# Kernel tuning notes

Measured on AMD Instinct MI355X. Metric: run time of the kernel, lower is better.

## Reference

```python
import jax, jax.numpy as jnp
import numpy as np

# ---- config (matches init_kwargs) ----
B, NP, DIM, HEADS, DH, NDIM = 32, 576, 512, 8, 64, 16
N = NP + 1                 # seq len incl cls token = 577
INNER = HEADS * DH         # 512


def setup_inputs() -> dict:
    key = jax.random.key(0)
    ks = jax.random.split(key, 11)
    D2 = 2 * DIM  # bidirectional EMA doubles kernel dim
    return {
        "x": jax.random.normal(ks[0], (B, N, DIM), jnp.float32),
        "W_qk": jax.random.normal(ks[1], (DIM, 2 * INNER), jnp.float32) / np.float32(np.sqrt(DIM)),
        "W_v": jax.random.normal(ks[2], (DIM, INNER), jnp.float32) / np.float32(np.sqrt(DIM)),
        "W_out": jax.random.normal(ks[3], (INNER, DIM), jnp.float32) / np.float32(np.sqrt(INNER)),
        "b_out": jnp.zeros((DIM,), jnp.float32),
        "rel_bias": jax.random.normal(ks[4], (2 * N - 1,), jnp.float32) * 0.02,
        "ema_delta": jax.random.normal(ks[5], (D2, NDIM, 1), jnp.float32),
        "ema_alpha": jax.random.normal(ks[6], (D2, NDIM, 1), jnp.float32),
        "ema_beta": jax.random.normal(ks[7], (D2, NDIM, 1), jnp.float32) * 0.5,
        "ema_gamma": jax.random.normal(ks[8], (D2, NDIM), jnp.float32) * 0.5,
        "ema_omega": jax.random.normal(ks[9], (DIM,), jnp.float32),
    }


def _ema_move(x, delta, alpha, beta, gamma, omega):
    """Bidirectional MultiHeadEMA (MEGA) via FFT convolution. x: (B, L, D)."""
    b, L, d = x.shape
    scale = jnp.asarray(np.sqrt(1.0 / NDIM), x.dtype)
    p = jax.nn.sigmoid(delta)                      # (2D, N, 1)
    q = 1.0 - p * jax.nn.sigmoid(alpha)            # (2D, N, 1), in (0,1)
    vander = jnp.arange(L, dtype=x.dtype)[None, None, :] * jnp.log(q)  # (2D, N, L)
    kern = (p * beta) * jnp.exp(vander)            # (2D, N, L)
    k = jnp.einsum('dnl,dn->dl', kern, gamma * scale)  # (2D, L)
    k1, k2 = k[:d], k[d:]
    # combined bidirectional kernel, length 2L-1
    kk = jnp.pad(k1, ((0, 0), (L - 1, 0))) + jnp.pad(k2[:, ::-1], ((0, 0), (0, L - 1)))
    xt = jnp.pad(x.transpose(0, 2, 1), ((0, 0), (0, 0), (L - 1, 0)))  # (B, D, 2L-1)
    fft_len = 2 * L - 1
    nfft = 2 * fft_len
    out = jnp.fft.irfft(jnp.fft.rfft(xt, n=nfft) * jnp.fft.rfft(kk, n=nfft)[None], n=nfft)
    s = 2 * L - 2
    out = out[..., s:s + L].transpose(0, 2, 1).astype(x.dtype)  # (B, L, D)
    return jax.nn.silu(out + x * omega)


def _rel_pos_bias(rb, seq_len):
    """RelativePositionalBias (MEGA): (2*N-1,) param -> (seq_len, seq_len) bias."""
    max_pos = N
    bvec = rb[max_pos - seq_len: max_pos + seq_len - 1]   # (2*seq_len-1,)
    t = jnp.pad(bvec, (0, seq_len))
    t = jnp.tile(t, seq_len)[:-seq_len].reshape(seq_len, 3 * seq_len - 2)
    r = (2 * seq_len - 1) // 2
    return t[:, r:t.shape[1] - r]


def reference(x, W_qk, W_v, W_out, b_out, rel_bias,
              ema_delta, ema_alpha, ema_beta, ema_gamma, ema_omega):
    b, n, _ = x.shape
    cls_tok = x[:, :1]
    moved = _ema_move(x[:, 1:], ema_delta, ema_alpha, ema_beta, ema_gamma, ema_omega)
    xm = jnp.concatenate([cls_tok, moved], axis=1)        # (B, N, DIM)
    q, k = jnp.split(xm @ W_qk, 2, axis=-1)
    v = xm @ W_v                                          # smooth_v_as_well=True

    def heads(t):
        return t.reshape(b, n, HEADS, DH).transpose(0, 2, 1, 3)  # (B, H, N, DH)

    q, k, v = heads(q), heads(k), heads(v)
    dots = jnp.einsum('bhid,bhjd->bhij', q, k) * (DH ** -0.5)
    attn = jax.nn.softmax(dots, axis=-1)
    attn = attn + _rel_pos_bias(rel_bias, n)[None, None]  # bias added AFTER softmax
    out = jnp.einsum('bhij,bhjd->bhid', attn, v)
    out = out.transpose(0, 2, 1, 3).reshape(b, n, INNER)
    return out @ W_out + b_out
```

## Files before the change

kernel.cpp:

```cpp
#include <hip/hip_runtime.h>

typedef unsigned short ushort;

typedef __bf16 bf16x8 __attribute__((ext_vector_type(8)));
typedef float  f32x4  __attribute__((ext_vector_type(4)));
typedef unsigned short u16x8 __attribute__((ext_vector_type(8)));
typedef unsigned short u16x4 __attribute__((ext_vector_type(4)));
typedef unsigned int   u32x2 __attribute__((ext_vector_type(2)));

static constexpr int BB   = 32;
static constexpr int NN   = 577;
static constexpr int LL   = 576;
static constexpr int DIMC = 512;
static constexpr int BN   = BB * NN;

static constexpr size_t SZ_WQKVT = 1536ull * 512 * 2;
static constexpr size_t SZ_WOUTT = 512ull * 512 * 2;
static constexpr size_t SZ_QK    = (size_t)BN * 1024 * 2;
static constexpr size_t SZ_V     = (size_t)BN * 512 * 2;
static constexpr size_t SZ_VT    = 256ull * 64 * 640 * 2;
static constexpr size_t OFF_WQKVT = 0;
static constexpr size_t OFF_WOUTT = OFF_WQKVT + SZ_WQKVT;
static constexpr size_t OFF_QTAB  = OFF_WOUTT + SZ_WOUTT;
static constexpr size_t OFF_CTAB  = OFF_QTAB + 65536;
static constexpr size_t OFF_QK    = OFF_CTAB + 65536;
static constexpr size_t OFF_V     = OFF_QK + SZ_QK;
static constexpr size_t OFF_REGION= OFF_V + SZ_V;
static constexpr size_t OFF_XM    = OFF_REGION;
static constexpr size_t OFF_VT    = OFF_REGION;
static constexpr size_t OFF_AO    = OFF_REGION + SZ_VT;
static constexpr size_t OFF_ST    = OFF_AO;
static constexpr size_t WS_NEEDED = OFF_AO + SZ_V;

__device__ __forceinline__ ushort bf16bits(float f) {
  unsigned int u = __builtin_bit_cast(unsigned int, f);
  u = (u + 0x7fffu + ((u >> 16) & 1u)) >> 16;
  return (ushort)u;
}
__device__ __forceinline__ float sigmoidf_(float z) { return 1.f / (1.f + __expf(-z)); }
__device__ __forceinline__ float siluf(float z)     { return z / (1.f + __expf(-z)); }

__global__ __launch_bounds__(256) void k_prep(
    const float* __restrict__ delta, const float* __restrict__ alpha,
    const float* __restrict__ beta,  const float* __restrict__ gamma,
    const float* __restrict__ Wqk,   const float* __restrict__ Wv,
    const float* __restrict__ Wout,
    float* __restrict__ qtab, float* __restrict__ ctab,
    ushort* __restrict__ Wqkvt, ushort* __restrict__ Woutt)
{
  int idx = blockIdx.x * 256 + threadIdx.x;
  if (idx < 16384) {
    float p = sigmoidf_(delta[idx]);
    float q = 1.f - p * sigmoidf_(alpha[idx]);
    qtab[idx] = q;
    ctab[idx] = p * beta[idx] * gamma[idx] * 0.25f;
  }
  int i2 = idx - 16384;
  if (i2 >= 0 && i2 < 1536 * 512) {
    int n = i2 >> 9, k = i2 & 511;
    float w = (n < 1024) ? Wqk[k * 1024 + n] : Wv[k * 512 + (n - 1024)];
    Wqkvt[i2] = bf16bits(w);
  }
  int i3 = i2 - 1536 * 512;
  if (i3 >= 0 && i3 < 512 * 512) {
    int n = i3 >> 9, k = i3 & 511;
    Woutt[i3] = bf16bits(Wout[k * 512 + n]);
  }
}


__global__ __launch_bounds__(64) void k_ema_p1(
    const float* __restrict__ x, const float* __restrict__ qtab,
    float* __restrict__ st)
{
  const int gx = blockIdx.x, cy = blockIdx.y, b = blockIdx.z;
  if (gx < 8) {
    const int d = gx * 64 + threadIdx.x;
    float q[16], h[16];
    #pragma unroll
    for (int n = 0; n < 16; ++n) { q[n] = qtab[d*16+n]; h[n] = 0.f; }
    const float* xp = x + ((size_t)b * NN + 1) * DIMC + d;
    const int blo = cy * 9;
    float xn[8];
    #pragma unroll
    for (int u = 0; u < 8; ++u) xn[u] = xp[(blo * 8 + u) * DIMC];
    for (int blk = blo; blk < blo + 9; ++blk) {
      float xv[8];
      #pragma unroll
      for (int u = 0; u < 8; ++u) xv[u] = xn[u];
      if (blk < blo + 8) {
        #pragma unroll
        for (int u = 0; u < 8; ++u) xn[u] = xp[((blk + 1) * 8 + u) * DIMC];
      }
      #pragma unroll
      for (int u = 0; u < 8; ++u) {
        float xx = xv[u];
        #pragma unroll
        for (int n = 0; n < 16; ++n) h[n] = fmaf(q[n], h[n], xx);
      }
    }
    float* sp = st + (((size_t)b * 8 + cy) * 16) * 512 + d;
    #pragma unroll
    for (int n = 0; n < 16; ++n) sp[n * 512] = h[n];
  } else {
    const int d = (gx - 8) * 64 + threadIdx.x;
    float q[16], g[16];
    #pragma unroll
    for (int n = 0; n < 16; ++n) { q[n] = qtab[(d+512)*16+n]; g[n] = 0.f; }
    const float* xp = x + ((size_t)b * NN + 1) * DIMC + d;
    const int blo = (7 - cy) * 9;
    float xn[8];
    #pragma unroll
    for (int u = 0; u < 8; ++u) xn[u] = xp[((blo + 8) * 8 + u) * DIMC];
    for (int blk = blo + 8; blk >= blo; --blk) {
      float xv[8];
      #pragma unroll
      for (int u = 0; u < 8; ++u) xv[u] = xn[u];
      if (blk > blo) {
        #pragma unroll
        for (int u = 0; u < 8; ++u) xn[u] = xp[((blk - 1) * 8 + u) * DIMC];
      }
      #pragma unroll
      for (int u = 7; u >= 0; --u) {
        float xx = xv[u];
        #pragma unroll
        for (int n = 0; n < 16; ++n) g[n] = fmaf(q[n], g[n], xx);
      }
    }
    float* sp = st + (((size_t)(32 + b) * 8 + cy) * 16) * 512 + d;
    #pragma unroll
    for (int n = 0; n < 16; ++n) sp[n * 512] = g[n];
  }
}

__global__ __launch_bounds__(256) void k_ema_mid(
    const float* __restrict__ qtab, float* __restrict__ st)
{
  int idx = blockIdx.x * 256 + threadIdx.x;
  int d = idx & 511;
  int rest = idx >> 9;
  int n = rest & 15;
  int db = rest >> 4;
  int dir = db >> 5;
  float q = qtab[(((size_t)dir << 9) + d) * 16 + n];
  float q2 = q * q, q4 = q2 * q2, q8 = q4 * q4;
  float q16 = q8 * q8, q32 = q16 * q16, q64 = q32 * q32;
  float qL = q64 * q8;
  float h = 0.f;
  float* sp = st + ((size_t)db * 128 + n) * 512 + d;
  #pragma unroll
  for (int c = 0; c < 8; ++c) {
    float tmp = (c < 7) ? sp[c * 8192] : 0.f;
    sp[c * 8192] = h;
    h = fmaf(qL, h, tmp);
  }
}

__global__ __launch_bounds__(64) void k_ema_p3(
    const float* __restrict__ x, const float* __restrict__ qtab,
    const float* __restrict__ ctab, const float* __restrict__ st,
    float* __restrict__ y1, float* __restrict__ y2)
{
  const int gx = blockIdx.x, cy = blockIdx.y, b = blockIdx.z;
  if (gx < 8) {
    const int d = gx * 64 + threadIdx.x;
    float q[16], c[16], h[16];
    const float* sp = st + (((size_t)b * 8 + cy) * 16) * 512 + d;
    #pragma unroll
    for (int n = 0; n < 16; ++n) { q[n] = qtab[d*16+n]; c[n] = ctab[d*16+n]; h[n] = sp[n*512]; }
    const float* xp = x  + ((size_t)b * NN + 1) * DIMC + d;
    float*       yp = y1 + ((size_t)b * LL)     * DIMC + d;
    const int blo = cy * 9;
    float xn[8];
    #pragma unroll
    for (int u = 0; u < 8; ++u) xn[u] = xp[(blo * 8 + u) * DIMC];
    for (int blk = blo; blk < blo + 9; ++blk) {
      float xv[8];
      #pragma unroll
      for (int u = 0; u < 8; ++u) xv[u] = xn[u];
      if (blk < blo + 8) {
        #pragma unroll
        for (int u = 0; u < 8; ++u) xn[u] = xp[((blk + 1) * 8 + u) * DIMC];
      }
      #pragma unroll
      for (int u = 0; u < 8; ++u) {
        float xx = xv[u], y = 0.f;
        #pragma unroll
        for (int n = 0; n < 16; ++n) { h[n] = fmaf(q[n], h[n], xx); y = fmaf(c[n], h[n], y); }
        yp[(blk * 8 + u) * DIMC] = y;
      }
    }
  } else {
    const int d = (gx - 8) * 64 + threadIdx.x;
    float q[16], c[16], g[16];
    const float* sp = st + (((size_t)(32 + b) * 8 + cy) * 16) * 512 + d;
    #pragma unroll
    for (int n = 0; n < 16; ++n) { q[n] = qtab[(d+512)*16+n]; c[n] = ctab[(d+512)*16+n]; g[n] = sp[n*512]; }
    const float* xp = x  + ((size_t)b * NN + 1) * DIMC + d;
    float*       yp = y2 + ((size_t)b * LL)     * DIMC + d;
    const int blo = (7 - cy) * 9;
    float xn[8];
    #pragma unroll
    for (int u = 0; u < 8; ++u) xn[u] = xp[((blo + 8) * 8 + u) * DIMC];
    for (int blk = blo + 8; blk >= blo; --blk) {
      float xv[8];
      #pragma unroll
      for (int u = 0; u < 8; ++u) xv[u] = xn[u];
      if (blk > blo) {
        #pragma unroll
        for (int u = 0; u < 8; ++u) xn[u] = xp[((blk - 1) * 8 + u) * DIMC];
      }
      #pragma unroll
      for (int u = 7; u >= 0; --u) {
        float xx = xv[u], y = 0.f;
        #pragma unroll
        for (int n = 0; n < 16; ++n) { g[n] = fmaf(q[n], g[n], xx); y = fmaf(c[n], g[n], y); }
        yp[(blk * 8 + u) * DIMC] = y;
      }
    }
  }
}

__global__ __launch_bounds__(256) void k_ema_comb(
    const float* __restrict__ x, const float* __restrict__ y1,
    const float* __restrict__ y2, const float* __restrict__ omega,
    ushort* __restrict__ xm)
{
  size_t v = (size_t)blockIdx.x * 256 + threadIdx.x;
  size_t e = v * 4;
  int n = (int)(e >> 9);
  int d = (int)(e & 511);
  int b = n / 577;
  int i = n - b * 577;
  f32x4 xv = *(const f32x4*)(x + e);
  u16x4 o;
  if (i == 0) {
    #pragma unroll
    for (int k = 0; k < 4; ++k) o[k] = bf16bits(xv[k]);
  } else {
    size_t ey = ((size_t)b * LL + (i - 1)) * DIMC + d;
    f32x4 a  = *(const f32x4*)(y1 + ey);
    f32x4 c2 = *(const f32x4*)(y2 + ey);
    f32x4 om = *(const f32x4*)(omega + d);
    #pragma unroll
    for (int k = 0; k < 4; ++k) o[k] = bf16bits(siluf(a[k] + c2[k] + xv[k] * om[k]));
  }
  *(u16x4*)(xm + e) = o;
}

__global__ __launch_bounds__(256) void k_qkv(
    const ushort* __restrict__ A, const ushort* __restrict__ Bt,
    ushort* __restrict__ qk, ushort* __restrict__ v)
{
  __shared__ alignas(16) ushort lA[128 * 40];
  __shared__ alignas(16) ushort lB[128 * 40];
  const int tid = threadIdx.x, wv = tid >> 6, lane = tid & 63;
  const int quad = lane >> 4, c16 = lane & 15;
  const int fid = blockIdx.y * 12 + blockIdx.x;
  const int xcd = fid & 7, ord = fid >> 3;
  const int wg  = (xcd < 4 ? xcd * 218 : 872 + (xcd - 4) * 217) + ord;
  const int row0 = (wg / 12) * 128, n0 = (wg % 12) * 128;
  const int wm = (wv >> 1) * 64, wn = (wv & 1) * 64;
  f32x4 z4 = {0.f, 0.f, 0.f, 0.f};
  f32x4 acc[4][4];
  #pragma unroll
  for (int mi = 0; mi < 4; ++mi)
    #pragma unroll
    for (int ni = 0; ni < 4; ++ni) acc[mi][ni] = z4;

  for (int kt = 0; kt < 16; ++kt) {
    const int k0 = kt * 32;
    u16x8 sa[2], sb[2];
    #pragma unroll
    for (int it = 0; it < 2; ++it) {
      int ch = it * 256 + tid;
      int r = ch >> 2, cc = ch & 3;
      int grow = row0 + r; if (grow > BN - 1) grow = BN - 1;
      sa[it] = *(const u16x8*)(A + (size_t)grow * 512 + k0 + cc * 8);
      sb[it] = *(const u16x8*)(Bt + (size_t)(n0 + r) * 512 + k0 + cc * 8);
    }
    __syncthreads();
    #pragma unroll
    for (int it = 0; it < 2; ++it) {
      int ch = it * 256 + tid;
      int r = ch >> 2, cc = ch & 3;
      *(u16x8*)(lA + r * 40 + cc * 8) = sa[it];
      *(u16x8*)(lB + r * 40 + cc * 8) = sb[it];
    }
    __syncthreads();
    bf16x8 af[4], bfv[4];
    #pragma unroll
    for (int mi = 0; mi < 4; ++mi)
      af[mi] = *(const bf16x8*)(lA + (wm + mi * 16 + c16) * 40 + quad * 8);
    #pragma unroll
    for (int ni = 0; ni < 4; ++ni)
      bfv[ni] = *(const bf16x8*)(lB + (wn + ni * 16 + c16) * 40 + quad * 8);
    #pragma unroll
    for (int mi = 0; mi < 4; ++mi)
      #pragma unroll
      for (int ni = 0; ni < 4; ++ni)
        acc[mi][ni] = __builtin_amdgcn_mfma_f32_16x16x32_bf16(af[mi], bfv[ni], acc[mi][ni], 0, 0, 0);
  }
  const bool isv = (n0 >= 1024);
  const float osc = (n0 < 512) ? 0.125f : 1.0f;
  #pragma unroll
  for (int mi = 0; mi < 4; ++mi) {
    #pragma unroll
    for (int r = 0; r < 4; ++r) {
      int grow = row0 + wm + mi * 16 + quad * 4 + r;
      if (grow < BN) {
        #pragma unroll
        for (int ni = 0; ni < 4; ++ni) {
          int col = n0 + wn + ni * 16 + c16;
          ushort vb = bf16bits(acc[mi][ni][r] * osc);
          if (!isv) qk[(size_t)grow * 1024 + col] = vb;
          else      v[(size_t)grow * 512 + (col - 1024)] = vb;
        }
      }
    }
  }
}

__global__ __launch_bounds__(256) void k_vtrans(
    const ushort* __restrict__ v, ushort* __restrict__ vt)
{
  __shared__ alignas(16) ushort lt[64 * 72];
  const int tid = threadIdx.x;
  const int bh = blockIdx.y, b = bh >> 3, h = bh & 7;
  const int j0 = blockIdx.x * 64;
  #pragma unroll
  for (int pass = 0; pass < 2; ++pass) {
    int cch = pass * 256 + tid;
    int jl = cch >> 3, cc = cch & 7;
    int gj = j0 + jl;
    u16x8 val = {0, 0, 0, 0, 0, 0, 0, 0};
    if (gj < 577) val = *(const u16x8*)(v + ((size_t)(b * NN + gj)) * 512 + h * 64 + cc * 8);
    *(u16x8*)(lt + jl * 72 + cc * 8) = val;
  }
  __syncthreads();
  #pragma unroll
  for (int pass = 0; pass < 2; ++pass) {
    int cch = pass * 256 + tid;
    int dh = cch >> 3, jc = cch & 7;
    u16x8 o;
    #pragma unroll
    for (int e = 0; e < 8; ++e) o[e] = lt[(jc * 8 + e) * 72 + dh];
    *(u16x8*)(vt + ((size_t)(bh * 64 + dh)) * 640 + j0 + jc * 8) = o;
  }
}

__global__ __launch_bounds__(256) void k_fattn(
    const ushort* __restrict__ qk, const ushort* __restrict__ vt,
    const float* __restrict__ relb, ushort* __restrict__ ao)
{
  __shared__ alignas(16) ushort lk[64 * 64];
  __shared__ alignas(16) ushort lv[64 * 64];
  __shared__ alignas(16) ushort lp[128 * 64];
  __shared__ ushort lbias16[1280];
  const int tid = threadIdx.x, wv = tid >> 6, lane = tid & 63;
  const int quad = lane >> 4, c16 = lane & 15;
  const int bh = blockIdx.x, b = bh >> 3, h = bh & 7;
  const int i0 = blockIdx.y * 128, wm = wv * 32;
  for (int t = tid; t < 1280; t += 256) {
    int idx = t - 64;
    lbias16[t] = (idx >= 0 && idx < 1153) ? bf16bits(relb[idx]) : (ushort)0;
  }
  bf16x8 aq[2][2];
  #pragma unroll
  for (int ms = 0; ms < 2; ++ms) {
    int gi = i0 + wm + ms * 16 + c16; if (gi > 576) gi = 576;
    const ushort* qp = qk + ((size_t)(b * NN + gi)) * 1024 + h * 64;
    #pragma unroll
    for (int kk = 0; kk < 2; ++kk)
      aq[ms][kk] = *(const bf16x8*)(qp + (kk * 4 + quad) * 8);
  }
  const int s_r = tid >> 3, s_c = tid & 7;
  const ushort* kbase = qk + ((size_t)b * NN) * 1024 + 512 + h * 64 + s_c * 8;
  const ushort* vbase = vt + ((size_t)bh * 64) * 640 + s_c * 8;

  float lsum[2] = {0.f, 0.f};
  f32x4 z4 = {0.f, 0.f, 0.f, 0.f};
  f32x4 accp[2][4], accb[2][4];
  #pragma unroll
  for (int ms = 0; ms < 2; ++ms)
    #pragma unroll
    for (int ns = 0; ns < 4; ++ns) { accp[ms][ns] = z4; accb[ms][ns] = z4; }

  u16x8 sk[2], sv[2];
  #pragma unroll
  for (int it = 0; it < 2; ++it) {
    int r = it * 32 + s_r;
    sk[it] = *(const u16x8*)(kbase + (size_t)r * 1024);
    sv[it] = *(const u16x8*)(vbase + (size_t)r * 640);
  }

  for (int jt = 0; jt < 10; ++jt) {
    __syncthreads();
    #pragma unroll
    for (int it = 0; it < 2; ++it) {
      int r = it * 32 + s_r;
      int pc = (s_c ^ (r & 7)) * 8;
      *(u16x8*)(lk + r * 64 + pc) = sk[it];
      *(u16x8*)(lv + r * 64 + pc) = sv[it];
    }
    __syncthreads();
    #pragma unroll
    for (int ms = 0; ms < 2; ++ms) {
      f32x4 dacc[4] = {z4, z4, z4, z4};
      #pragma unroll
      for (int kk = 0; kk < 2; ++kk) {
        const int ck = kk * 4 + quad;
        #pragma unroll
        for (int ns = 0; ns < 4; ++ns) {
          const int row = ns * 16 + c16;
          bf16x8 bk = *(const bf16x8*)(lk + row * 64 + ((ck ^ (row & 7)) * 8));
          dacc[ns] = __builtin_amdgcn_mfma_f32_16x16x32_bf16(bk, aq[ms][kk], dacc[ns], 0, 0, 0);
        }
      }
      const int irow = wm + ms * 16 + c16;
      const int xr = irow & 7;
      #pragma unroll
      for (int ns = 0; ns < 4; ++ns) {
        float ex[4];
        #pragma unroll
        for (int r = 0; r < 4; ++r) {
          float e = __expf(dacc[ns][r]);
          if (jt == 9 && (ns * 16 + quad * 4 + r) >= 1) e = 0.f;
          ex[r] = e;
        }
        lsum[ms] += (ex[0] + ex[1]) + (ex[2] + ex[3]);
        unsigned int p0 = (unsigned int)bf16bits(ex[0]) | ((unsigned int)bf16bits(ex[1]) << 16);
        unsigned int p1 = (unsigned int)bf16bits(ex[2]) | ((unsigned int)bf16bits(ex[3]) << 16);
        u32x2 pw = {p0, p1};
        const int lc = ns * 2 + (quad >> 1);
        *(u32x2*)(lp + irow * 64 + ((lc ^ xr) * 8) + (quad & 1) * 4) = pw;
      }
    }
    __syncthreads();
    if (jt < 9) {
      const int j0n = (jt + 1) * 64;
      #pragma unroll
      for (int it = 0; it < 2; ++it) {
        int r = it * 32 + s_r;
        int gj = j0n + r; if (gj > 576) gj = 576;
        sk[it] = *(const u16x8*)(kbase + (size_t)gj * 1024);
        sv[it] = *(const u16x8*)(vbase + (size_t)r * 640 + j0n);
      }
    }
    const int j0 = jt * 64;
    #pragma unroll
    for (int kk = 0; kk < 2; ++kk) {
      const int ck = kk * 4 + quad;
      bf16x8 ap[2], ab[2];
      #pragma unroll
      for (int ms = 0; ms < 2; ++ms) {
        const int row = wm + ms * 16 + c16;
        ap[ms] = *(const bf16x8*)(lp + row * 64 + ((ck ^ (row & 7)) * 8));
        u16x8 abu;
        const int base = 64 + 576 + j0 + kk * 32 + quad * 8 - (i0 + row);
        #pragma unroll
        for (int e = 0; e < 8; ++e) abu[e] = lbias16[base + e];
        ab[ms] = __builtin_bit_cast(bf16x8, abu);
      }
      #pragma unroll
      for (int ns = 0; ns < 4; ++ns) {
        const int row = ns * 16 + c16;
        bf16x8 bV = *(const bf16x8*)(lv + row * 64 + ((ck ^ (row & 7)) * 8));
        #pragma unroll
        for (int ms = 0; ms < 2; ++ms) {
          accp[ms][ns] = __builtin_amdgcn_mfma_f32_16x16x32_bf16(ap[ms], bV, accp[ms][ns], 0, 0, 0);
          accb[ms][ns] = __builtin_amdgcn_mfma_f32_16x16x32_bf16(ab[ms], bV, accb[ms][ns], 0, 0, 0);
        }
      }
    }
  }
  float tot[2];
  #pragma unroll
  for (int ms = 0; ms < 2; ++ms) {
    float t = lsum[ms];
    t += __shfl_xor(t, 16);
    t += __shfl_xor(t, 32);
    tot[ms] = t;
  }
  #pragma unroll
  for (int ms = 0; ms < 2; ++ms) {
    #pragma unroll
    for (int r = 0; r < 4; ++r) {
      float li = 1.f / __shfl(tot[ms], quad * 4 + r);
      int ii = i0 + wm + ms * 16 + quad * 4 + r;
      if (ii < 577) {
        #pragma unroll
        for (int ns = 0; ns < 4; ++ns)
          ao[((size_t)(b * NN + ii)) * 512 + h * 64 + ns * 16 + c16] =
              bf16bits(accp[ms][ns][r] * li + accb[ms][ns][r]);
      }
    }
  }
}

__global__ __launch_bounds__(256) void k_out(
    const ushort* __restrict__ A, const ushort* __restrict__ Bt,
    const float* __restrict__ bout, float* __restrict__ out)
{
  __shared__ alignas(16) ushort lA[128 * 40];
  __shared__ alignas(16) ushort lB[128 * 40];
  const int tid = threadIdx.x, wv = tid >> 6, lane = tid & 63;
  const int quad = lane >> 4, c16 = lane & 15;
  const int row0 = blockIdx.y * 128, n0 = blockIdx.x * 128;
  const int wm = (wv >> 1) * 64, wn = (wv & 1) * 64;
  f32x4 z4 = {0.f, 0.f, 0.f, 0.f};
  f32x4 acc[4][4];
  #pragma unroll
  for (int mi = 0; mi < 4; ++mi)
    #pragma unroll
    for (int ni = 0; ni < 4; ++ni) acc[mi][ni] = z4;

  for (int kt = 0; kt < 16; ++kt) {
    const int k0 = kt * 32;
    u16x8 sa[2], sb[2];
    #pragma unroll
    for (int it = 0; it < 2; ++it) {
      int ch = it * 256 + tid;
      int r = ch >> 2, cc = ch & 3;
      int grow = row0 + r; if (grow > BN - 1) grow = BN - 1;
      sa[it] = *(const u16x8*)(A + (size_t)grow * 512 + k0 + cc * 8);
      sb[it] = *(const u16x8*)(Bt + (size_t)(n0 + r) * 512 + k0 + cc * 8);
    }
    __syncthreads();
    #pragma unroll
    for (int it = 0; it < 2; ++it) {
      int ch = it * 256 + tid;
      int r = ch >> 2, cc = ch & 3;
      *(u16x8*)(lA + r * 40 + cc * 8) = sa[it];
      *(u16x8*)(lB + r * 40 + cc * 8) = sb[it];
    }
    __syncthreads();
    bf16x8 af[4], bfv[4];
    #pragma unroll
    for (int mi = 0; mi < 4; ++mi)
      af[mi] = *(const bf16x8*)(lA + (wm + mi * 16 + c16) * 40 + quad * 8);
    #pragma unroll
    for (int ni = 0; ni < 4; ++ni)
      bfv[ni] = *(const bf16x8*)(lB + (wn + ni * 16 + c16) * 40 + quad * 8);
    #pragma unroll
    for (int mi = 0; mi < 4; ++mi)
      #pragma unroll
      for (int ni = 0; ni < 4; ++ni)
        acc[mi][ni] = __builtin_amdgcn_mfma_f32_16x16x32_bf16(af[mi], bfv[ni], acc[mi][ni], 0, 0, 0);
  }
  #pragma unroll
  for (int mi = 0; mi < 4; ++mi) {
    #pragma unroll
    for (int r = 0; r < 4; ++r) {
      int grow = row0 + wm + mi * 16 + quad * 4 + r;
      if (grow < BN) {
        #pragma unroll
        for (int ni = 0; ni < 4; ++ni) {
          int col = n0 + wn + ni * 16 + c16;
          out[(size_t)grow * 512 + col] = acc[mi][ni][r] + bout[col];
        }
      }
    }
  }
}

extern "C" void kernel_launch(void* const* d_in, const int* in_sizes, int n_in,
                              void* d_out, int out_size, void* d_ws, size_t ws_size,
                              hipStream_t stream) {
  (void)in_sizes; (void)n_in; (void)out_size;
  if (ws_size < WS_NEEDED) return;
  const float* x    = (const float*)d_in[0];
  const float* Wqk  = (const float*)d_in[1];
  const float* Wv   = (const float*)d_in[2];
  const float* Wout = (const float*)d_in[3];
  const float* bout = (const float*)d_in[4];
  const float* relb = (const float*)d_in[5];
  const float* edel = (const float*)d_in[6];
  const float* ealp = (const float*)d_in[7];
  const float* ebet = (const float*)d_in[8];
  const float* egam = (const float*)d_in[9];
  const float* eome = (const float*)d_in[10];

  char* ws = (char*)d_ws;
  ushort* Wqkvt = (ushort*)(ws + OFF_WQKVT);
  ushort* Woutt = (ushort*)(ws + OFF_WOUTT);
  float*  qtab  = (float*)(ws + OFF_QTAB);
  float*  ctab  = (float*)(ws + OFF_CTAB);
  ushort* qkb   = (ushort*)(ws + OFF_QK);
  ushort* vb    = (ushort*)(ws + OFF_V);
  ushort* xm    = (ushort*)(ws + OFF_XM);
  ushort* vtb   = (ushort*)(ws + OFF_VT);
  ushort* aob   = (ushort*)(ws + OFF_AO);
  float*  stf   = (float*)(ws + OFF_ST);
  float*  outp  = (float*)d_out;
  float*  y1    = outp;
  float*  y2    = (float*)(ws + OFF_QK);

  k_prep<<<dim3(4160), dim3(256), 0, stream>>>(edel, ealp, ebet, egam, Wqk, Wv, Wout,
                                               qtab, ctab, Wqkvt, Woutt);
  k_ema_p1<<<dim3(16, 7, 32), dim3(64), 0, stream>>>(x, qtab, stf);
  k_ema_mid<<<dim3(2048), dim3(256), 0, stream>>>(qtab, stf);
  k_ema_p3<<<dim3(16, 8, 32), dim3(64), 0, stream>>>(x, qtab, ctab, stf, y1, y2);
  k_ema_comb<<<dim3(9232), dim3(256), 0, stream>>>(x, y1, y2, eome, xm);
  k_qkv<<<dim3(12, 145), dim3(256), 0, stream>>>(xm, Wqkvt, qkb, vb);
  k_vtrans<<<dim3(10, 256), dim3(256), 0, stream>>>(vb, vtb);
  k_fattn<<<dim3(256, 5), dim3(256), 0, stream>>>(qkb, vtb, relb, aob);
  k_out<<<dim3(4, 145), dim3(256), 0, stream>>>(aob, Woutt, bout, outp);
}
```

Baseline: 324.6 us.

## Fuse bidirectional EMA scans with combine step and use exp2 softmax

Merges the forward and backward EMA scan kernel with the combine kernel. Each block now runs the backward scan into an fp16 shared buffer, then runs the forward scan and writes silu(y1+y2+x*omega) straight to bf16 xm. This removes the fp32 y1/y2 round trip through global memory and one launch, but halves the block count, serialises the two scans inside each block, and stores one scan direction in fp16. It also folds log2(e) into the Q scale so the attention kernel can use exp2, and moves the next K/V tile prefetch earlier, dropping one barrier.

```diff
diff --git a/kernel.cpp b/kernel.cpp
--- a/kernel.cpp
+++ b/kernel.cpp
@@ -156,29 +156,65 @@
   }
 }
 
-__global__ __launch_bounds__(64) void k_ema_p3(
+__global__ __launch_bounds__(64) void k_ema_fuse(
     const float* __restrict__ x, const float* __restrict__ qtab,
     const float* __restrict__ ctab, const float* __restrict__ st,
-    float* __restrict__ y1, float* __restrict__ y2)
-{
+    const float* __restrict__ omega, ushort* __restrict__ xm)
+{
+  __shared__ _Float16 yb[72 * 64];
+  const int lane = threadIdx.x;
   const int gx = blockIdx.x, cy = blockIdx.y, b = blockIdx.z;
-  if (gx < 8) {
-    const int d = gx * 64 + threadIdx.x;
+  const int d = gx * 64 + lane;
+  const float* xp = x + ((size_t)b * NN + 1 + cy * 72) * DIMC + d;
+  {
+    float q[16], c[16], g[16];
+    const float* sp = st + (((size_t)(32 + b) * 8 + (7 - cy)) * 16) * 512 + d;
+    #pragma unroll
+    for (int n = 0; n < 16; ++n) {
+      q[n] = qtab[(d + 512) * 16 + n];
+      c[n] = ctab[(d + 512) * 16 + n];
+      g[n] = sp[n * 512];
+    }
+    float xn[8];
+    #pragma unroll
+    for (int u = 0; u < 8; ++u) xn[u] = xp[(64 + u) * DIMC];
+    for (int blk = 8; blk >= 0; --blk) {
+      float xv[8];
+      #pragma unroll
+      for (int u = 0; u < 8; ++u) xv[u] = xn[u];
+      if (blk > 0) {
+        #pragma unroll
+        for (int u = 0; u < 8; ++u) xn[u] = xp[((blk - 1) * 8 + u) * DIMC];
+      }
+      #pragma unroll
+      for (int u = 7; u >= 0; --u) {
+        float xx = xv[u], y = 0.f;
+        #pragma unroll
+        for (int n = 0; n < 16; ++n) { g[n] = fmaf(q[n], g[n], xx); y = fmaf(c[n], g[n], y); }
+        yb[(blk * 8 + u) * 64 + lane] = (_Float16)y;
+      }
+    }
+  }
+  __syncthreads();
+  {
     float q[16], c[16], h[16];
     const float* sp = st + (((size_t)b * 8 + cy) * 16) * 512 + d;
     #pragma unroll
-    for (int n = 0; n < 16; ++n) { q[n] = qtab[d*16+n]; c[n] = ctab[d*16+n]; h[n] = sp[n*512]; }
-    const float* xp = x  + ((size_t)b * NN + 1) * DIMC + d;
-    float*       yp = y1 + ((size_t)b * LL)     * DIMC + d;
-    const int blo = cy * 9;
+    for (int n = 0; n < 16; ++n) {
+      q[n] = qtab[d * 16 + n];
+      c[n] = ctab[d * 16 + n];
+      h[n] = sp[n * 512];
+    }
+    const float om = omega[d];
+    ushort* op = xm + ((size_t)b * NN + 1 + cy * 72) * DIMC + d;
     float xn[8];
     #pragma unroll
-    for (int u = 0; u < 8; ++u) xn[u] = xp[(blo * 8 + u) * DIMC];
-    for (int blk = blo; blk < blo + 9; ++blk) {
+    for (int u = 0; u < 8; ++u) xn[u] = xp[u * DIMC];
+    for (int blk = 0; blk < 9; ++blk) {
       float xv[8];
       #pragma unroll
       for (int u = 0; u < 8; ++u) xv[u] = xn[u];
-      if (blk < blo + 8) {
+      if (blk < 8) {
         #pragma unroll
         for (int u = 0; u < 8; ++u) xn[u] = xp[((blk + 1) * 8 + u) * DIMC];
       }
@@ -187,65 +223,15 @@
         float xx = xv[u], y = 0.f;
         #pragma unroll
         for (int n = 0; n < 16; ++n) { h[n] = fmaf(q[n], h[n], xx); y = fmaf(c[n], h[n], y); }
-        yp[(blk * 8 + u) * DIMC] = y;
-      }
-    }
-  } else {
-    const int d = (gx - 8) * 64 + threadIdx.x;
-    float q[16], c[16], g[16];
-    const float* sp = st + (((size_t)(32 + b) * 8 + cy) * 16) * 512 + d;
-    #pragma unroll
-    for (int n = 0; n < 16; ++n) { q[n] = qtab[(d+512)*16+n]; c[n] = ctab[(d+512)*16+n]; g[n] = sp[n*512]; }
-    const float* xp = x  + ((size_t)b * NN + 1) * DIMC + d;
-    float*       yp = y2 + ((size_t)b * LL)     * DIMC + d;
-    const int blo = (7 - cy) * 9;
-    float xn[8];
-    #pragma unroll
-    for (int u = 0; u < 8; ++u) xn[u] = xp[((blo + 8) * 8 + u) * DIMC];
-    for (int blk = blo + 8; blk >= blo; --blk) {
-      float xv[8];
-      #pragma unroll
-      for (int u = 0; u < 8; ++u) xv[u] = xn[u];
-      if (blk > blo) {
-        #pragma unroll
-        for (int u = 0; u < 8; ++u) xn[u] = xp[((blk - 1) * 8 + u) * DIMC];
-      }
-      #pragma unroll
-      for (int u = 7; u >= 0; --u) {
-        float xx = xv[u], y = 0.f;
-        #pragma unroll
-        for (int n = 0; n < 16; ++n) { g[n] = fmaf(q[n], g[n], xx); y = fmaf(c[n], g[n], y); }
-        yp[(blk * 8 + u) * DIMC] = y;
-      }
-    }
-  }
-}
-
-__global__ __launch_bounds__(256) void k_ema_comb(
-    const float* __restrict__ x, const float* __restrict__ y1,
-    const float* __restrict__ y2, const float* __restrict__ omega,
-    ushort* __restrict__ xm)
-{
-  size_t v = (size_t)blockIdx.x * 256 + threadIdx.x;
-  size_t e = v * 4;
-  int n = (int)(e >> 9);
-  int d = (int)(e & 511);
-  int b = n / 577;
-  int i = n - b * 577;
-  f32x4 xv = *(const f32x4*)(x + e);
-  u16x4 o;
-  if (i == 0) {
-    #pragma unroll
-    for (int k = 0; k < 4; ++k) o[k] = bf16bits(xv[k]);
-  } else {
-    size_t ey = ((size_t)b * LL + (i - 1)) * DIMC + d;
-    f32x4 a  = *(const f32x4*)(y1 + ey);
-    f32x4 c2 = *(const f32x4*)(y2 + ey);
-    f32x4 om = *(const f32x4*)(omega + d);
-    #pragma unroll
-    for (int k = 0; k < 4; ++k) o[k] = bf16bits(siluf(a[k] + c2[k] + xv[k] * om[k]));
-  }
-  *(u16x4*)(xm + e) = o;
+        float s = y + (float)yb[(blk * 8 + u) * 64 + lane] + xx * om;
+        op[(blk * 8 + u) * DIMC] = bf16bits(siluf(s));
+      }
+    }
+  }
+  if (cy == 0) {
+    size_t e0 = ((size_t)b * NN) * DIMC + d;
+    xm[e0] = bf16bits(x[e0]);
+  }
 }
 
 __global__ __launch_bounds__(256) void k_qkv(
@@ -302,7 +288,7 @@
         acc[mi][ni] = __builtin_amdgcn_mfma_f32_16x16x32_bf16(af[mi], bfv[ni], acc[mi][ni], 0, 0, 0);
   }
   const bool isv = (n0 >= 1024);
-  const float osc = (n0 < 512) ? 0.125f : 1.0f;
+  const float osc = (n0 < 512) ? 0.1803368801111f : 1.0f;
   #pragma unroll
   for (int mi = 0; mi < 4; ++mi) {
     #pragma unroll
@@ -404,6 +390,16 @@
       *(u16x8*)(lv + r * 64 + pc) = sv[it];
     }
     __syncthreads();
+    if (jt < 9) {
+      const int j0n = (jt + 1) * 64;
+      #pragma unroll
+      for (int it = 0; it < 2; ++it) {
+        int r = it * 32 + s_r;
+        int gj = j0n + r; if (gj > 576) gj = 576;
+        sk[it] = *(const u16x8*)(kbase + (size_t)gj * 1024);
+        sv[it] = *(const u16x8*)(vbase + (size_t)r * 640 + j0n);
+      }
+    }
     #pragma unroll
     for (int ms = 0; ms < 2; ++ms) {
       f32x4 dacc[4] = {z4, z4, z4, z4};
@@ -424,7 +420,7 @@
         float ex[4];
         #pragma unroll
         for (int r = 0; r < 4; ++r) {
-          float e = __expf(dacc[ns][r]);
+          float e = __builtin_amdgcn_exp2f(dacc[ns][r]);
           if (jt == 9 && (ns * 16 + quad * 4 + r) >= 1) e = 0.f;
           ex[r] = e;
         }
@@ -434,17 +430,6 @@
         u32x2 pw = {p0, p1};
         const int lc = ns * 2 + (quad >> 1);
         *(u32x2*)(lp + irow * 64 + ((lc ^ xr) * 8) + (quad & 1) * 4) = pw;
-      }
-    }
-    __syncthreads();
-    if (jt < 9) {
-      const int j0n = (jt + 1) * 64;
-      #pragma unroll
-      for (int it = 0; it < 2; ++it) {
-        int r = it * 32 + s_r;
-        int gj = j0n + r; if (gj > 576) gj = 576;
-        sk[it] = *(const u16x8*)(kbase + (size_t)gj * 1024);
-        sv[it] = *(const u16x8*)(vbase + (size_t)r * 640 + j0n);
       }
     }
     const int j0 = jt * 64;
@@ -593,15 +578,12 @@
   ushort* aob   = (ushort*)(ws + OFF_AO);
   float*  stf   = (float*)(ws + OFF_ST);
   float*  outp  = (float*)d_out;
-  float*  y1    = outp;
-  float*  y2    = (float*)(ws + OFF_QK);
 
   k_prep<<<dim3(4160), dim3(256), 0, stream>>>(edel, ealp, ebet, egam, Wqk, Wv, Wout,
                                                qtab, ctab, Wqkvt, Woutt);
   k_ema_p1<<<dim3(16, 7, 32), dim3(64), 0, stream>>>(x, qtab, stf);
   k_ema_mid<<<dim3(2048), dim3(256), 0, stream>>>(qtab, stf);
-  k_ema_p3<<<dim3(16, 8, 32), dim3(64), 0, stream>>>(x, qtab, ctab, stf, y1, y2);
-  k_ema_comb<<<dim3(9232), dim3(256), 0, stream>>>(x, y1, y2, eome, xm);
+  k_ema_fuse<<<dim3(8, 8, 32), dim3(64), 0, stream>>>(x, qtab, ctab, stf, eome, xm);
   k_qkv<<<dim3(12, 145), dim3(256), 0, stream>>>(xm, Wqkvt, qkb, vb);
   k_vtrans<<<dim3(10, 256), dim3(256), 0, stream>>>(vb, vtb);
   k_fattn<<<dim3(256, 5), dim3(256), 0, stream>>>(qkb, vtb, relb, aob);
```

Measured after the change: 306.4 us. 5.6% less time.
